# Kernel tuning notes

Measured on AMD Instinct MI355X. Metric: run time of the kernel, lower is better.

## Reference

```python
import jax, jax.numpy as jnp
import numpy as np

NFE = 8            # round(time / step_size) = round(1.0 / 0.125)
STEP = 0.125


def setup_inputs() -> dict:
    key = jax.random.key(0)
    k1, k2, k3 = jax.random.split(key, 3)
    N, C, V, L = 64, 64, 500, 12
    x = jax.random.normal(k1, (N, C, V, L), dtype=jnp.float32)
    # random adjacency, row-normalized (typical diffusion operator; keeps Euler stable)
    adj = jax.random.uniform(k2, (V, V), dtype=jnp.float32)
    adj = adj / jnp.sum(adj, axis=1, keepdims=True)
    in_total = (NFE + 1) * C  # 576
    out_dim = 64
    W = jax.random.normal(k3, (out_dim, in_total), dtype=jnp.float32) * (1.0 / np.sqrt(in_total))
    b = jnp.zeros((out_dim,), dtype=jnp.float32)
    return {"x": x, "adj": adj, "W": W, "b": b}


def reference(x, adj, W, b):
    # Euler integration of dx/dt = A x over the node dim:
    # out[n,c,v,l] = sum_w x[n,c,w,l] * A[v,w]
    states = [x]
    cur = x
    for _ in range(NFE):  # fixed, small step count
        ax = jnp.einsum('ncwl,vw->ncvl', cur, adj)
        cur = cur + STEP * ax
        states.append(cur)
    h = jnp.concatenate(states, axis=1)  # [N, (NFE+1)*C, V, L]
    # 1x1 Conv2d == channel GEMM
    out = jnp.einsum('ncvl,oc->novl', h, W) + b[None, :, None, None]
    return out
```

## Files before the change

kernel.cpp:

```cpp
#include <hip/hip_runtime.h>
#include <hip/hip_bf16.h>
#include <stdint.h>

typedef __attribute__((ext_vector_type(8))) short short8;
typedef __attribute__((ext_vector_type(4))) short short4v;
typedef __attribute__((ext_vector_type(4))) float f32x4;
typedef __attribute__((ext_vector_type(4))) float fvec4;

__device__ __forceinline__ short f2bf(float f) {
  unsigned u = __builtin_bit_cast(unsigned, f);
  unsigned r = u + 0x7fffu + ((u >> 16) & 1u);
  return (short)(r >> 16);
}

__device__ __forceinline__ void gload_lds16(const void* g, void* l) {
  __builtin_amdgcn_global_load_lds(
      (const __attribute__((address_space(1))) void*)g,
      (__attribute__((address_space(3))) void*)l, 16, 0, 0);
}

#define VP   512
#define TILE_SHORTS 8192
#define PANEL_TILES 72
#define NSTEP 65

__device__ __forceinline__ int tswz(int r, int c) {
  return r * 64 + ((((c >> 3) ^ (r & 7)) << 3) | (c & 7));
}

__global__ __launch_bounds__(256) void initM_kernel(const float* __restrict__ adj,
    float* __restrict__ Mpow, short* __restrict__ Mt, short* __restrict__ M1T) {
  int idx = blockIdx.x * 256 + threadIdx.x;
  int v = idx >> 9, w = idx & 511;
  float m = 0.f;
  if (v < 500 && w < 500) m = 0.125f * adj[v * 500 + w] + (v == w ? 1.f : 0.f);
  Mpow[idx] = m;
  M1T[(size_t)w * VP + v] = f2bf(m);
  int bx = v >> 7, r = v & 127, c = w & 63;
  int kt0 = (w >> 6), kt1 = 8 + (w >> 6);
  Mt[(size_t)(bx * PANEL_TILES + kt0) * TILE_SHORTS + tswz(r, c)] =
      f2bf((v == w && v < 500) ? 1.f : 0.f);
  Mt[(size_t)(bx * PANEL_TILES + kt1) * TILE_SHORTS + tswz(r, c)] = f2bf(m);
}

__global__ __launch_bounds__(256) void wprep_kernel(const float* __restrict__ W,
    short* __restrict__ Wbf) {
  int idx = blockIdx.x * 256 + threadIdx.x;
  int e = idx & 7, l4 = (idx >> 3) & 15, h = (idx >> 7) & 3;
  int ks = (idx >> 9) & 1, jm = (idx >> 10) & 3, k = idx >> 12;
  int o = jm * 16 + l4, c = k * 64 + ks * 32 + h * 8 + e;
  Wbf[idx] = f2bf(W[o * 576 + c]);
}

__global__ __launch_bounds__(256) void powstep_kernel(const float* __restrict__ src,
    const short* __restrict__ M1T, float* __restrict__ dst,
    short* __restrict__ Mt, int kslice) {
  int tid = threadIdx.x, wv = tid >> 6, lane = tid & 63;
  int tile = blockIdx.x * 4 + wv;
  int tv = tile >> 5, tw = tile & 31;
  int row  = tv * 16 + (lane & 15);
  int colw = tw * 16 + (lane & 15);
  int kgrp = (lane >> 4) * 8;
  const short* mcol = M1T + (size_t)colw * VP;
  f32x4 acc = {0.f, 0.f, 0.f, 0.f};
  for (int k0 = 0; k0 < 512; k0 += 32) {
    int kc = k0 + kgrp;
    fvec4 f0 = *(const fvec4*)&src[row * VP + kc];
    fvec4 f1 = *(const fvec4*)&src[row * VP + kc + 4];
    short8 a;
    for (int t = 0; t < 4; ++t) { a[t] = f2bf(f0[t]); a[4 + t] = f2bf(f1[t]); }
    short8 b = *(const short8*)&mcol[kc];
    acc = __builtin_amdgcn_mfma_f32_16x16x32_bf16(a, b, acc, 0, 0, 0);
  }
  for (int r = 0; r < 4; ++r) {
    int i = (lane >> 4) * 4 + r;
    int vv = tv * 16 + i;
    float val = acc[r];
    dst[vv * VP + colw] = val;
    int bx = vv >> 7, rr = vv & 127, c = colw & 63;
    int kt = kslice * 8 + (colw >> 6);
    Mt[(size_t)(bx * PANEL_TILES + kt) * TILE_SHORTS + tswz(rr, c)] = f2bf(val);
  }
}

__global__ __launch_bounds__(256) void xpose_kernel(const float* __restrict__ x,
    short* __restrict__ xb) {
  int t = threadIdx.x, wv = t >> 6, lane = t & 63;
  int p  = blockIdx.x & 1;
  int w0 = (blockIdx.x >> 1) * 64;
  int n  = blockIdx.y;
  const float* xs = x + (size_t)n * 64 * 6000;
  __shared__ short xl[32 * 770];
  for (int ci = 0; ci < 8; ++ci) {
    int crow = wv * 8 + ci;
    int c = p * 32 + crow;
    for (int i = 0; i < 3; ++i) {
      int wl = (i * 64 + lane) * 4;
      int gwl = w0 * 12 + wl;
      fvec4 v = {0.f, 0.f, 0.f, 0.f};
      if (gwl + 3 < 6000) {
        v = *(const fvec4*)&xs[(size_t)c * 6000 + gwl];
      } else {
        for (int e = 0; e < 4; ++e)
          if (gwl + e < 6000) v[e] = xs[(size_t)c * 6000 + gwl + e];
      }
      for (int e = 0; e < 4; ++e) xl[crow * 770 + wl + e] = f2bf(v[e]);
    }
  }
  __syncthreads();
  for (int i = 0; i < 12; ++i) {
    int ct = i * 256 + t;
    int bl = ct & 3;
    int w_l = (ct >> 2) & 63;
    int l = ct >> 8;
    short8 s;
    for (int j = 0; j < 8; ++j)
      s[j] = xl[(bl * 8 + j) * 770 + w_l * 12 + l];
    size_t dst = ((size_t)(n * 12 + l) * 512 + w0 + w_l) * 64 + (p * 4 + bl) * 8;
    *(short8*)(xb + dst) = s;
  }
}

__global__ __launch_bounds__(256) void zbuild_kernel(const short* __restrict__ xb,
    const short* __restrict__ Wbf, short* __restrict__ Zt, int n0) {
  int t = threadIdx.x, wv = t >> 6, lane = t & 63;
  int bxx = blockIdx.x;
  int jh = bxx & 1;
  int lh = bxx >> 1;
  int l = lh >> 1, wh = lh & 1;
  int nloc = blockIdx.y;
  int n = n0 + nloc;
  const short* xbase = xb + (size_t)(n * 12 + l) * 512 * 64;
  short8 af[4][2];
  for (int q = 0; q < 4; ++q)
    for (int ks = 0; ks < 2; ++ks) {
      int wrow = wh * 256 + wv * 64 + q * 16 + (lane & 15);
      int cblk = ks * 4 + (lane >> 4);
      af[q][ks] = *(const short8*)(xbase + (size_t)wrow * 64 + cblk * 8);
    }
  int lanebase = (lane & 15) * 12 + l;
  int kt_off = wh * 4 + wv;
  const short* wbase = Wbf + (lane >> 4) * 128 + (lane & 15) * 8;
  for (int j = jh * 18; j < jh * 18 + 18; ++j) {
    int k = j >> 2, jm = j & 3;
    const short* wp = wbase + (size_t)((k * 4 + jm) * 2) * 512;
    short8 bw0 = *(const short8*)(wp);
    short8 bw1 = *(const short8*)(wp + 512);
    f32x4 acc[4];
    for (int q = 0; q < 4; ++q) {
      acc[q] = (f32x4){0.f, 0.f, 0.f, 0.f};
      acc[q] = __builtin_amdgcn_mfma_f32_16x16x32_bf16(af[q][0], bw0, acc[q], 0, 0, 0);
      acc[q] = __builtin_amdgcn_mfma_f32_16x16x32_bf16(af[q][1], bw1, acc[q], 0, 0, 0);
    }
    int zr = jm * 192 + lanebase;
    int pr = zr >> 7, rr = zr & 127;
    size_t tbase = ((size_t)(nloc * 6 + pr) * PANEL_TILES + k * 8 + kt_off) * TILE_SHORTS
                 + rr * 64;
    for (int q = 0; q < 4; ++q) {
      int c4 = q * 16 + (lane >> 4) * 4;
      size_t idx = tbase + ((((c4 >> 3) ^ (zr & 7)) << 3) | (c4 & 7));
      short4v s;
      for (int e = 0; e < 4; ++e) s[e] = f2bf(acc[q][e]);
      *(short4v*)(Zt + idx) = s;
    }
  }
}

__global__ __launch_bounds__(256) void biggemm_kernel(const short* __restrict__ Zt,
    const short* __restrict__ Mt, const float* __restrict__ bvec,
    float* __restrict__ out, int n0) {
  int tid = threadIdx.x, wv = tid >> 6, lane = tid & 63;
  int nwg = gridDim.x;
  int b = blockIdx.x;
  int swz = (b & 7) * (nwg >> 3) + (b >> 3);
  int bx = swz & 7;
  int rest = swz >> 3;
  int by = rest % 6;
  int bz = rest / 6;
  int v0    = bx * 64;
  int rowM0 = by * 128;
  int n = n0 + bz;
  __shared__ short As[2][TILE_SHORTS];
  __shared__ short Bs[2][TILE_SHORTS / 2];
  f32x4 acc[2][4];
  for (int i = 0; i < 2; ++i)
    for (int j = 0; j < 4; ++j) acc[i][j] = (f32x4){0.f, 0.f, 0.f, 0.f};
  const char* Apanel = (const char*)(Zt + (size_t)(bz * 6 + by) * PANEL_TILES * TILE_SHORTS);
  const char* Bpanel = (const char*)(Mt + (size_t)(bx >> 1) * PANEL_TILES * TILE_SHORTS)
                     + (bx & 1) * 8192;

  auto ktmap = [&](int s) { return (s == 0) ? bx : (s + 7); };

  auto STAGE = [&](int p, int kt) {
    const char* a  = Apanel + (size_t)kt * (TILE_SHORTS * 2);
    const char* bb = Bpanel + (size_t)kt * (TILE_SHORTS * 2);
#pragma unroll
    for (int cc = 0; cc < 4; ++cc) {
      int chunk = cc * 4 + wv;
      int off = chunk * 1024 + lane * 16;
      gload_lds16(a + off, (char*)As[p] + chunk * 1024);
    }
#pragma unroll
    for (int cc = 0; cc < 2; ++cc) {
      int chunk = cc * 4 + wv;
      int off = chunk * 1024 + lane * 16;
      gload_lds16(bb + off, (char*)Bs[p] + chunk * 1024);
    }
  };

  STAGE(0, ktmap(0));
  STAGE(1, ktmap(1));

  for (int s = 0; s < NSTEP; ++s) {
    int d = s & 1;
    if (s < NSTEP - 1) {
      asm volatile("s_waitcnt vmcnt(6)" ::: "memory");
    } else {
      asm volatile("s_waitcnt vmcnt(0)" ::: "memory");
    }
    __builtin_amdgcn_sched_barrier(0);
    __builtin_amdgcn_s_barrier();

    short8 af[2][2], bf[2][4];
#pragma unroll
    for (int kk = 0; kk < 2; ++kk) {
      int cbyte = kk * 64 + (lane >> 4) * 16;
#pragma unroll
      for (int mi = 0; mi < 2; ++mi) {
        int r = wv * 32 + mi * 16 + (lane & 15);
        af[kk][mi] = *(const short8*)((const char*)As[d] + r * 128 + (cbyte ^ ((r & 7) << 4)));
      }
#pragma unroll
      for (int ni = 0; ni < 4; ++ni) {
        int r2 = ni * 16 + (lane & 15);
        bf[kk][ni] = *(const short8*)((const char*)Bs[d] + r2 * 128 + (cbyte ^ ((r2 & 7) << 4)));
      }
    }
    asm volatile("s_waitcnt lgkmcnt(0)" ::: "memory");
    __builtin_amdgcn_sched_barrier(0);
    __builtin_amdgcn_s_barrier();

    if (s + 2 < NSTEP) STAGE(d, ktmap(s + 2));

    __builtin_amdgcn_s_setprio(1);
#pragma unroll
    for (int kk = 0; kk < 2; ++kk)
#pragma unroll
      for (int mi = 0; mi < 2; ++mi)
#pragma unroll
        for (int ni = 0; ni < 4; ++ni)
          acc[mi][ni] = __builtin_amdgcn_mfma_f32_16x16x32_bf16(af[kk][mi], bf[kk][ni],
                                                                acc[mi][ni], 0, 0, 0);
    __builtin_amdgcn_s_setprio(0);
  }

  for (int mi = 0; mi < 2; ++mi) {
    for (int r = 0; r < 4; ++r) {
      int gm = rowM0 + wv * 32 + mi * 16 + (lane >> 4) * 4 + r;
      int o = gm / 12, l = gm - o * 12;
      float bo = bvec[o];
      size_t obase = (((size_t)n * 64 + o) * 500) * 12 + l;
      for (int ni = 0; ni < 4; ++ni) {
        int v = v0 + ni * 16 + (lane & 15);
        if (v < 500) out[obase + (size_t)v * 12] = acc[mi][ni][r] + bo;
      }
    }
  }
}

extern "C" void kernel_launch(void* const* d_in, const int* in_sizes, int n_in,
                              void* d_out, int out_size, void* d_ws, size_t ws_size,
                              hipStream_t stream) {
  const float* x   = (const float*)d_in[0];
  const float* adj = (const float*)d_in[1];
  const float* W   = (const float*)d_in[2];
  const float* bv  = (const float*)d_in[3];
  float* out = (float*)d_out;
  char* ws = (char*)d_ws;

  size_t off = 0;
  float* Mpow0 = (float*)(ws + off); off += (size_t)512 * 512 * 4;
  float* Mpow1 = (float*)(ws + off); off += (size_t)512 * 512 * 4;
  short* M1T   = (short*)(ws + off); off += (size_t)512 * 512 * 2;
  short* Wbf   = (short*)(ws + off); off += (size_t)36864 * 2;
  short* Mt    = (short*)(ws + off); off += (size_t)4 * PANEL_TILES * TILE_SHORTS * 2;
  short* xb    = (short*)(ws + off); off += (size_t)64 * 12 * 512 * 64 * 2;
  short* Zt    = (short*)(ws + off);
  size_t per_n = (size_t)6 * PANEL_TILES * TILE_SHORTS * 2;
  int nchunk = 1;
  if (ws_size > off) {
    size_t a = (ws_size - off) / per_n;
    nchunk = (a >= 16) ? 16 : (a < 1 ? 1 : (int)a);
  }

  hipLaunchKernelGGL(initM_kernel, dim3(1024), dim3(256), 0, stream, adj, Mpow0, Mt, M1T);
  hipLaunchKernelGGL(wprep_kernel, dim3(144), dim3(256), 0, stream, W, Wbf);
  const float* src = Mpow0; float* dst = Mpow1;
  for (int k = 2; k <= 8; ++k) {
    hipLaunchKernelGGL(powstep_kernel, dim3(256), dim3(256), 0, stream, src, M1T, dst, Mt, k);
    float* t = dst; dst = (float*)src; src = t;
  }
  hipLaunchKernelGGL(xpose_kernel, dim3(16, 64), dim3(256), 0, stream, x, xb);
  for (int n0 = 0; n0 < 64; n0 += nchunk) {
    int cn = (64 - n0) < nchunk ? (64 - n0) : nchunk;
    hipLaunchKernelGGL(zbuild_kernel, dim3(48, cn), dim3(256), 0, stream, xb, Wbf, Zt, n0);
    hipLaunchKernelGGL(biggemm_kernel, dim3(48 * cn), dim3(256), 0, stream, Zt, Mt, bv, out, n0);
  }
}
```

Before: 507.6 us.

## Process two batch samples per GEMM workgroup to reuse the B tile

Each biggemm workgroup now computes two batch items that share the same Mt (B) tile, loading two A panels and one B panel per step and issuing twice the MFMAs. This halves B-tile global traffic and LDS B loads per unit of output, and halves the grid size. In exchange, LDS use grows to about 80KB per block and the accumulator registers double, which may reduce occupancy. The chunk count is also forced to be even.

```diff
diff --git a/kernel.cpp b/kernel.cpp
--- a/kernel.cpp
+++ b/kernel.cpp
@@ -166,7 +166,7 @@
   }
 }
 
-__global__ __launch_bounds__(256) void biggemm_kernel(const short* __restrict__ Zt,
+__global__ __launch_bounds__(256, 2) void biggemm_kernel(const short* __restrict__ Zt,
     const short* __restrict__ Mt, const float* __restrict__ bvec,
     float* __restrict__ out, int n0) {
   int tid = threadIdx.x, wv = tid >> 6, lane = tid & 63;
@@ -176,29 +176,37 @@
   int bx = swz & 7;
   int rest = swz >> 3;
   int by = rest % 6;
-  int bz = rest / 6;
+  int bzp = rest / 6;
   int v0    = bx * 64;
   int rowM0 = by * 128;
-  int n = n0 + bz;
-  __shared__ short As[2][TILE_SHORTS];
+  int n1 = n0 + bzp * 2;
+  int n2 = n1 + 1;
+  __shared__ short As1[2][TILE_SHORTS];
+  __shared__ short As2[2][TILE_SHORTS];
   __shared__ short Bs[2][TILE_SHORTS / 2];
-  f32x4 acc[2][4];
+  f32x4 acc1[2][4], acc2[2][4];
   for (int i = 0; i < 2; ++i)
-    for (int j = 0; j < 4; ++j) acc[i][j] = (f32x4){0.f, 0.f, 0.f, 0.f};
-  const char* Apanel = (const char*)(Zt + (size_t)(bz * 6 + by) * PANEL_TILES * TILE_SHORTS);
+    for (int j = 0; j < 4; ++j) {
+      acc1[i][j] = (f32x4){0.f, 0.f, 0.f, 0.f};
+      acc2[i][j] = (f32x4){0.f, 0.f, 0.f, 0.f};
+    }
+  const char* Apanel1 = (const char*)(Zt + (size_t)((bzp * 2)     * 6 + by) * PANEL_TILES * TILE_SHORTS);
+  const char* Apanel2 = (const char*)(Zt + (size_t)((bzp * 2 + 1) * 6 + by) * PANEL_TILES * TILE_SHORTS);
   const char* Bpanel = (const char*)(Mt + (size_t)(bx >> 1) * PANEL_TILES * TILE_SHORTS)
                      + (bx & 1) * 8192;
 
   auto ktmap = [&](int s) { return (s == 0) ? bx : (s + 7); };
 
   auto STAGE = [&](int p, int kt) {
-    const char* a  = Apanel + (size_t)kt * (TILE_SHORTS * 2);
-    const char* bb = Bpanel + (size_t)kt * (TILE_SHORTS * 2);
+    const char* a1 = Apanel1 + (size_t)kt * (TILE_SHORTS * 2);
+    const char* a2 = Apanel2 + (size_t)kt * (TILE_SHORTS * 2);
+    const char* bb = Bpanel  + (size_t)kt * (TILE_SHORTS * 2);
 #pragma unroll
     for (int cc = 0; cc < 4; ++cc) {
       int chunk = cc * 4 + wv;
       int off = chunk * 1024 + lane * 16;
-      gload_lds16(a + off, (char*)As[p] + chunk * 1024);
+      gload_lds16(a1 + off, (char*)As1[p] + chunk * 1024);
+      gload_lds16(a2 + off, (char*)As2[p] + chunk * 1024);
     }
 #pragma unroll
     for (int cc = 0; cc < 2; ++cc) {
@@ -214,21 +222,23 @@
   for (int s = 0; s < NSTEP; ++s) {
     int d = s & 1;
     if (s < NSTEP - 1) {
-      asm volatile("s_waitcnt vmcnt(6)" ::: "memory");
+      asm volatile("s_waitcnt vmcnt(10)" ::: "memory");
     } else {
       asm volatile("s_waitcnt vmcnt(0)" ::: "memory");
     }
     __builtin_amdgcn_sched_barrier(0);
     __builtin_amdgcn_s_barrier();
 
-    short8 af[2][2], bf[2][4];
+    short8 af1[2][2], af2[2][2], bf[2][4];
 #pragma unroll
     for (int kk = 0; kk < 2; ++kk) {
       int cbyte = kk * 64 + (lane >> 4) * 16;
 #pragma unroll
       for (int mi = 0; mi < 2; ++mi) {
         int r = wv * 32 + mi * 16 + (lane & 15);
-        af[kk][mi] = *(const short8*)((const char*)As[d] + r * 128 + (cbyte ^ ((r & 7) << 4)));
+        int o8 = r * 128 + (cbyte ^ ((r & 7) << 4));
+        af1[kk][mi] = *(const short8*)((const char*)As1[d] + o8);
+        af2[kk][mi] = *(const short8*)((const char*)As2[d] + o8);
       }
 #pragma unroll
       for (int ni = 0; ni < 4; ++ni) {
@@ -248,9 +258,12 @@
 #pragma unroll
       for (int mi = 0; mi < 2; ++mi)
 #pragma unroll
-        for (int ni = 0; ni < 4; ++ni)
-          acc[mi][ni] = __builtin_amdgcn_mfma_f32_16x16x32_bf16(af[kk][mi], bf[kk][ni],
-                                                                acc[mi][ni], 0, 0, 0);
+        for (int ni = 0; ni < 4; ++ni) {
+          acc1[mi][ni] = __builtin_amdgcn_mfma_f32_16x16x32_bf16(af1[kk][mi], bf[kk][ni],
+                                                                 acc1[mi][ni], 0, 0, 0);
+          acc2[mi][ni] = __builtin_amdgcn_mfma_f32_16x16x32_bf16(af2[kk][mi], bf[kk][ni],
+                                                                 acc2[mi][ni], 0, 0, 0);
+        }
     __builtin_amdgcn_s_setprio(0);
   }
 
@@ -259,10 +272,14 @@
       int gm = rowM0 + wv * 32 + mi * 16 + (lane >> 4) * 4 + r;
       int o = gm / 12, l = gm - o * 12;
       float bo = bvec[o];
-      size_t obase = (((size_t)n * 64 + o) * 500) * 12 + l;
+      size_t ob1 = (((size_t)n1 * 64 + o) * 500) * 12 + l;
+      size_t ob2 = (((size_t)n2 * 64 + o) * 500) * 12 + l;
       for (int ni = 0; ni < 4; ++ni) {
         int v = v0 + ni * 16 + (lane & 15);
-        if (v < 500) out[obase + (size_t)v * 12] = acc[mi][ni][r] + bo;
+        if (v < 500) {
+          out[ob1 + (size_t)v * 12] = acc1[mi][ni][r] + bo;
+          out[ob2 + (size_t)v * 12] = acc2[mi][ni][r] + bo;
+        }
       }
     }
   }
@@ -287,10 +304,12 @@
   short* xb    = (short*)(ws + off); off += (size_t)64 * 12 * 512 * 64 * 2;
   short* Zt    = (short*)(ws + off);
   size_t per_n = (size_t)6 * PANEL_TILES * TILE_SHORTS * 2;
-  int nchunk = 1;
+  int nchunk = 2;
   if (ws_size > off) {
     size_t a = (ws_size - off) / per_n;
-    nchunk = (a >= 16) ? 16 : (a < 1 ? 1 : (int)a);
+    nchunk = (a >= 16) ? 16 : (a < 2 ? 2 : (int)a);
+    nchunk &= ~1;
+    if (nchunk < 2) nchunk = 2;
   }
 
   hipLaunchKernelGGL(initM_kernel, dim3(1024), dim3(256), 0, stream, adj, Mpow0, Mt, M1T);
@@ -304,6 +323,6 @@
   for (int n0 = 0; n0 < 64; n0 += nchunk) {
     int cn = (64 - n0) < nchunk ? (64 - n0) : nchunk;
     hipLaunchKernelGGL(zbuild_kernel, dim3(48, cn), dim3(256), 0, stream, xb, Wbf, Zt, n0);
-    hipLaunchKernelGGL(biggemm_kernel, dim3(48 * cn), dim3(256), 0, stream, Zt, Mt, bv, out, n0);
-  }
-}
+    hipLaunchKernelGGL(biggemm_kernel, dim3(24 * cn), dim3(256), 0, stream, Zt, Mt, bv, out, n0);
+  }
+}
```

After: 508.6 us. No clear change (+0.2%).
